# Kernel optimization log

Measured on AMD Instinct MI355X. Metric: run time of the kernel, lower is better.

Reference implementation:

```python
import jax, jax.numpy as jnp
import numpy as np

DIM = 512
LEAF_DIM = 128
DEPTH = 3
NUM_LEAVES = 2 ** DEPTH  # 8
B, T = 4, 2048


def setup_inputs() -> dict:
    key = jax.random.key(0)
    ks = jax.random.split(key, 16)
    sD = DIM ** -0.5
    sF = LEAF_DIM ** -0.5
    inp = {
        "inputs": jax.random.normal(ks[0], (B, T, DIM), jnp.float32),
        "training": 1,
    }
    # per-level node (routing) params: (D, 2^d)
    for d in range(DEPTH):
        n = 2 ** d
        inp[f"wn{d}"] = jax.random.normal(ks[1 + d], (DIM, n), jnp.float32) * sD
        inp[f"bn{d}"] = jnp.zeros((n,), jnp.float32)
    # stacked leaf FFN params
    inp["w1a"] = jax.random.normal(ks[8], (NUM_LEAVES, DIM, LEAF_DIM), jnp.float32) * sD
    inp["b1a"] = jnp.zeros((NUM_LEAVES, LEAF_DIM), jnp.float32)
    inp["w1b"] = jax.random.normal(ks[9], (NUM_LEAVES, DIM, LEAF_DIM), jnp.float32) * sD
    inp["b1b"] = jnp.zeros((NUM_LEAVES, LEAF_DIM), jnp.float32)
    inp["w2"] = jax.random.normal(ks[10], (NUM_LEAVES, LEAF_DIM, DIM), jnp.float32) * sF
    inp["b2"] = jnp.zeros((NUM_LEAVES, DIM), jnp.float32)
    return inp


def reference(inputs, training, wn0, bn0, wn1, bn1, wn2, bn2, w1a, b1a, w1b, b1b, w2, b2):
    Bs, Ts, D = inputs.shape
    L = NUM_LEAVES
    sg = jax.lax.stop_gradient
    mixture = jnp.ones((Bs, Ts, L), inputs.dtype)
    for wn, bn in ((wn0, bn0), (wn1, bn1), (wn2, bn2)):
        n = wn.shape[1]  # nodes at this depth
        c = jax.nn.sigmoid(inputs @ wn + bn)  # (B,T,n)
        if training:
            # straight-through hard rounding
            c = c - sg(c) + sg(jnp.rint(c))
        else:
            c = jnp.rint(c)
        c_nc = jnp.stack([c, 1.0 - c], -1).reshape(Bs, Ts, 2 * n, 1)
        mixture = (mixture.reshape(Bs, Ts, 2 * n, L // (2 * n)) * c_nc)
    mixture = mixture.reshape(Bs, Ts, L)
    # dense per-leaf gated FFN, masked by mixture
    h = (jnp.einsum('btd,ldf->btlf', inputs, w1a) + b1a) * \
        (jnp.einsum('btd,ldf->btlf', inputs, w1b) + b1b)  # (B,T,L,F)
    y2 = jnp.einsum('btlf,lfd->btld', h, w2) + b2          # (B,T,L,D)
    y = (y2 * mixture[..., None]).sum(-2)                  # (B,T,D)
    return y
```

## Files before the change

### kernel.cpp

```cpp
#include <hip/hip_runtime.h>
#include <hip/hip_bf16.h>

#define N_TOK 8192
#define DIM   512
#define FDIM  128
#define BM    32

typedef __attribute__((ext_vector_type(8))) short short8;
typedef __attribute__((ext_vector_type(4))) float floatx4;

__device__ inline short f2bf(float f) {
    union { float f; unsigned u; } v; v.f = f;
    unsigned r = (v.u + 0x7FFF + ((v.u >> 16) & 1)) >> 16;
    return (short)r;
}

__global__ __launch_bounds__(256) void k_prep(
    const float* __restrict__ x,
    const float* __restrict__ wn0, const float* __restrict__ bn0,
    const float* __restrict__ wn1, const float* __restrict__ bn1,
    const float* __restrict__ wn2, const float* __restrict__ bn2,
    const float* __restrict__ w1a, const float* __restrict__ w1b,
    const float* __restrict__ w2,
    int* __restrict__ counts, int* __restrict__ lists,
    short* __restrict__ pw1a, short* __restrict__ pw1b, short* __restrict__ pw2,
    short* __restrict__ xbf)
{
    const int blk = blockIdx.x;
    if (blk < 128) {
        __shared__ int leafs[64];
        const int t = threadIdx.x;
        const int wave = t >> 6, lane = t & 63;
        const int d0 = lane * 8;
        float v0[8], v1[16], v2[32];
        #pragma unroll
        for (int j = 0; j < 8; ++j)  v0[j] = wn0[d0 + j];
        #pragma unroll
        for (int j = 0; j < 16; ++j) v1[j] = wn1[d0 * 2 + j];
        #pragma unroll
        for (int j = 0; j < 32; ++j) v2[j] = wn2[d0 * 4 + j];
        const float b0s = bn0[0];
        const float b1s[2] = {bn1[0], bn1[1]};
        const float b2s[4] = {bn2[0], bn2[1], bn2[2], bn2[3]};
        for (int i = 0; i < 16; ++i) {
            const int tok = blk * 64 + wave * 16 + i;
            const float4* xp = (const float4*)(x + tok * DIM + d0);
            const float4 xa = xp[0], xb = xp[1];
            const float xv[8] = {xa.x, xa.y, xa.z, xa.w, xb.x, xb.y, xb.z, xb.w};
            short8 xo;
            #pragma unroll
            for (int j = 0; j < 8; ++j) xo[j] = f2bf(xv[j]);
            *(short8*)(xbf + (size_t)tok * DIM + d0) = xo;
            float a0 = 0.f, a1[2] = {0.f, 0.f}, a2[4] = {0.f, 0.f, 0.f, 0.f};
            #pragma unroll
            for (int j = 0; j < 8; ++j) {
                a0    += xv[j] * v0[j];
                a1[0] += xv[j] * v1[j * 2];     a1[1] += xv[j] * v1[j * 2 + 1];
                a2[0] += xv[j] * v2[j * 4];     a2[1] += xv[j] * v2[j * 4 + 1];
                a2[2] += xv[j] * v2[j * 4 + 2]; a2[3] += xv[j] * v2[j * 4 + 3];
            }
            #pragma unroll
            for (int off = 32; off >= 1; off >>= 1) {
                a0    += __shfl_xor(a0, off, 64);
                a1[0] += __shfl_xor(a1[0], off, 64);
                a1[1] += __shfl_xor(a1[1], off, 64);
                a2[0] += __shfl_xor(a2[0], off, 64);
                a2[1] += __shfl_xor(a2[1], off, 64);
                a2[2] += __shfl_xor(a2[2], off, 64);
                a2[3] += __shfl_xor(a2[3], off, 64);
            }
            int p = (a0 + b0s > 0.f) ? 0 : 1;
            const float t1 = a1[p] + b1s[p];
            p = p * 2 + ((t1 > 0.f) ? 0 : 1);
            const float t2 = a2[p] + b2s[p];
            p = p * 2 + ((t2 > 0.f) ? 0 : 1);
            if (lane == 0) leafs[wave * 16 + i] = p;
        }
        __syncthreads();
        if (t < 8) {
            const int l = t;
            int c = 0;
            for (int i = 0; i < 64; ++i) c += (leafs[i] == l);
            if (c > 0) {
                int base = atomicAdd(counts + l * 16, c);
                int j = 0;
                for (int i = 0; i < 64; ++i)
                    if (leafs[i] == l) lists[l * N_TOK + base + (j++)] = blk * 64 + i;
            }
        }
    } else {
        const int wid  = (blk - 128) * 4 + (threadIdx.x >> 6);
        const int lane = threadIdx.x & 63;
        const int q = lane >> 4, m = lane & 15;
        if (wid < 2048) {
            const float* src = (wid < 1024) ? w1a : w1b;
            short*       dst = (wid < 1024) ? pw1a : pw1b;
            const int f = wid & 1023;
            const int l = f >> 7, kb = (f >> 3) & 15, nt = f & 7;
            const float* s = src + l * 65536 + (kb * 32 + q * 8) * FDIM + nt * 16 + m;
            short8 o;
            #pragma unroll
            for (int j = 0; j < 8; ++j) o[j] = f2bf(s[j * FDIM]);
            *(short8*)(dst + f * 512 + lane * 8) = o;
        } else {
            const int f = wid - 2048;
            const int l = f >> 7, kb = (f >> 5) & 3, nt = f & 31;
            const float* s = w2 + l * 65536 + (kb * 32 + q * 8) * DIM + nt * 16 + m;
            short8 o;
            #pragma unroll
            for (int j = 0; j < 8; ++j) o[j] = f2bf(s[j * DIM]);
            *(short8*)(pw2 + f * 512 + lane * 8) = o;
        }
    }
}

__global__ __launch_bounds__(512, 4) void k_ffn(
    const short* __restrict__ xbf,
    const float* __restrict__ b1a, const float* __restrict__ b1b,
    const float* __restrict__ b2,
    const short* __restrict__ pw1a, const short* __restrict__ pw1b,
    const short* __restrict__ pw2,
    const int* __restrict__ counts, const int* __restrict__ lists,
    float* __restrict__ out)
{
    const int leaf = blockIdx.y;
    const int tile = blockIdx.x;
    const int cnt  = counts[leaf * 16];
    if (tile * BM >= cnt) return;

    __shared__ int   toks[BM];
    __shared__ short xs[BM][DIM + 8];
    __shared__ short hs[BM][FDIM + 8];

    const int t = threadIdx.x;
    if (t < BM) {
        const int idx = tile * BM + t;
        toks[t] = lists[leaf * N_TOK + ((idx < cnt) ? idx : cnt - 1)];
    }
    __syncthreads();

    {
        const int row = t >> 4, c0 = (t & 15) * 32;
        const short8* src = (const short8*)(xbf + (size_t)toks[row] * DIM + c0);
        const short8 s0 = src[0], s1 = src[1], s2 = src[2], s3 = src[3];
        short8* dst = (short8*)&xs[row][c0];
        dst[0] = s0; dst[1] = s1; dst[2] = s2; dst[3] = s3;
    }
    __syncthreads();

    const int wave = t >> 6, lane = t & 63;
    const int qd = lane >> 4, mm = lane & 15;

    floatx4 aA0 = {0,0,0,0}, aA1 = {0,0,0,0}, aB0 = {0,0,0,0}, aB1 = {0,0,0,0};
    const short* pa = pw1a + ((leaf * 16) * 8 + wave) * 512 + lane * 8;
    const short* pb = pw1b + ((leaf * 16) * 8 + wave) * 512 + lane * 8;
    #pragma unroll
    for (int kb = 0; kb < 16; ++kb) {
        const short8 af0 = *(const short8*)&xs[mm][kb * 32 + qd * 8];
        const short8 af1 = *(const short8*)&xs[16 + mm][kb * 32 + qd * 8];
        const short8 ba  = *(const short8*)(pa + kb * (8 * 512));
        const short8 bb  = *(const short8*)(pb + kb * (8 * 512));
        aA0 = __builtin_amdgcn_mfma_f32_16x16x32_bf16(af0, ba, aA0, 0, 0, 0);
        aA1 = __builtin_amdgcn_mfma_f32_16x16x32_bf16(af1, ba, aA1, 0, 0, 0);
        aB0 = __builtin_amdgcn_mfma_f32_16x16x32_bf16(af0, bb, aB0, 0, 0, 0);
        aB1 = __builtin_amdgcn_mfma_f32_16x16x32_bf16(af1, bb, aB1, 0, 0, 0);
    }
    {
        const int c0 = wave * 16 + mm;
        const float ba_ = b1a[leaf * FDIM + c0];
        const float bb_ = b1b[leaf * FDIM + c0];
        #pragma unroll
        for (int r = 0; r < 4; ++r) {
            const int r0 = qd * 4 + r;
            hs[r0][c0]      = f2bf((aA0[r] + ba_) * (aB0[r] + bb_));
            hs[16 + r0][c0] = f2bf((aA1[r] + ba_) * (aB1[r] + bb_));
        }
    }
    __syncthreads();

    floatx4 acc[8];
    #pragma unroll
    for (int j = 0; j < 8; ++j) acc[j] = (floatx4){0, 0, 0, 0};
    #pragma unroll
    for (int kb = 0; kb < 4; ++kb) {
        const short8 af0 = *(const short8*)&hs[mm][kb * 32 + qd * 8];
        const short8 af1 = *(const short8*)&hs[16 + mm][kb * 32 + qd * 8];
        #pragma unroll
        for (int j = 0; j < 4; ++j) {
            const int nt = wave * 4 + j;
            const short8 bf = *(const short8*)(pw2 + (((leaf * 4 + kb) * 32 + nt) * 512) + lane * 8);
            acc[j * 2]     = __builtin_amdgcn_mfma_f32_16x16x32_bf16(af0, bf, acc[j * 2],     0, 0, 0);
            acc[j * 2 + 1] = __builtin_amdgcn_mfma_f32_16x16x32_bf16(af1, bf, acc[j * 2 + 1], 0, 0, 0);
        }
    }
    const int rem = cnt - tile * BM;
    #pragma unroll
    for (int j = 0; j < 4; ++j) {
        const int col = (wave * 4 + j) * 16 + mm;
        const float bias = b2[leaf * DIM + col];
        #pragma unroll
        for (int r = 0; r < 4; ++r) {
            const int r0 = qd * 4 + r;
            if (r0 < rem)      out[toks[r0] * DIM + col]      = acc[j * 2][r]     + bias;
            if (16 + r0 < rem) out[toks[16 + r0] * DIM + col] = acc[j * 2 + 1][r] + bias;
        }
    }
}

extern "C" void kernel_launch(void* const* d_in, const int* in_sizes, int n_in,
                              void* d_out, int out_size, void* d_ws, size_t ws_size,
                              hipStream_t stream) {
    const float* x   = (const float*)d_in[0];
    const float* wn0 = (const float*)d_in[2];
    const float* bn0 = (const float*)d_in[3];
    const float* wn1 = (const float*)d_in[4];
    const float* bn1 = (const float*)d_in[5];
    const float* wn2 = (const float*)d_in[6];
    const float* bn2 = (const float*)d_in[7];
    const float* w1a = (const float*)d_in[8];
    const float* b1a = (const float*)d_in[9];
    const float* w1b = (const float*)d_in[10];
    const float* b1b = (const float*)d_in[11];
    const float* w2  = (const float*)d_in[12];
    const float* b2  = (const float*)d_in[13];
    float* out = (float*)d_out;

    char* ws = (char*)d_ws;
    int*   counts = (int*)(ws);
    int*   lists  = (int*)(ws + 512);
    short* pw1a   = (short*)(ws + 262656);
    short* pw1b   = (short*)(ws + 262656 + 1048576);
    short* pw2    = (short*)(ws + 262656 + 2097152);
    short* xbf    = (short*)(ws + 262656 + 3145728);

    hipMemsetAsync(counts, 0, 512, stream);
    k_prep<<<896, 256, 0, stream>>>(x, wn0, bn0, wn1, bn1, wn2, bn2,
                                    w1a, w1b, w2, counts, lists, pw1a, pw1b, pw2, xbf);
    k_ffn<<<dim3(256, 8), 512, 0, stream>>>(xbf, b1a, b1b, b2, pw1a, pw1b, pw2,
                                            counts, lists, out);
}
```

Baseline: 135.7 us.

## Fuse routing prep and leaf FFN into one cooperative persistent kernel

Merges the prep kernel (routing, bf16 conversion, weight packing) and the FFN kernel into a single cooperative launch of 256 blocks. A grid-wide sync separates the two phases. The FFN phase then pulls tiles from an atomic work queue instead of launching a sparse 256x8 grid with many early-exit blocks. This removes one kernel launch and the idle blocks, but adds grid-sync cost, queue atomics, and a lower occupancy bound of 2 blocks per CU.

```diff
diff --git a/kernel.cpp b/kernel.cpp
--- a/kernel.cpp
+++ b/kernel.cpp
@@ -1,5 +1,7 @@
 #include <hip/hip_runtime.h>
-#include <hip/hip_bf16.h>
+#include <hip/hip_cooperative_groups.h>
+
+namespace cg = cooperative_groups;
 
 #define N_TOK 8192
 #define DIM   512
@@ -15,22 +17,31 @@
     return (short)r;
 }
 
-__global__ __launch_bounds__(256) void k_prep(
+__global__ __launch_bounds__(512, 2) void k_fused(
     const float* __restrict__ x,
     const float* __restrict__ wn0, const float* __restrict__ bn0,
     const float* __restrict__ wn1, const float* __restrict__ bn1,
     const float* __restrict__ wn2, const float* __restrict__ bn2,
     const float* __restrict__ w1a, const float* __restrict__ w1b,
     const float* __restrict__ w2,
-    int* __restrict__ counts, int* __restrict__ lists,
+    const float* __restrict__ b1a, const float* __restrict__ b1b,
+    const float* __restrict__ b2,
+    int* __restrict__ counts, int* __restrict__ lists, int* __restrict__ queue,
     short* __restrict__ pw1a, short* __restrict__ pw1b, short* __restrict__ pw2,
-    short* __restrict__ xbf)
+    short* __restrict__ xbf,
+    float* __restrict__ out)
 {
-    const int blk = blockIdx.x;
-    if (blk < 128) {
-        __shared__ int leafs[64];
-        const int t = threadIdx.x;
-        const int wave = t >> 6, lane = t & 63;
+    const int blk  = blockIdx.x;
+    const int t    = threadIdx.x;
+    const int wave = t >> 6, lane = t & 63;
+
+    __shared__ int   sleafs[32];
+    __shared__ int   toks[BM];
+    __shared__ short xs[BM][DIM + 8];
+    __shared__ short hs[BM][FDIM + 8];
+    __shared__ int   s_it;
+
+    if (wave < 4) {
         const int d0 = lane * 8;
         float v0[8], v1[16], v2[32];
         #pragma unroll
@@ -42,8 +53,9 @@
         const float b0s = bn0[0];
         const float b1s[2] = {bn1[0], bn1[1]};
         const float b2s[4] = {bn2[0], bn2[1], bn2[2], bn2[3]};
-        for (int i = 0; i < 16; ++i) {
-            const int tok = blk * 64 + wave * 16 + i;
+        #pragma unroll 2
+        for (int i = 0; i < 8; ++i) {
+            const int tok = blk * 32 + wave * 8 + i;
             const float4* xp = (const float4*)(x + tok * DIM + d0);
             const float4 xa = xp[0], xb = xp[1];
             const float xv[8] = {xa.x, xa.y, xa.z, xa.w, xb.x, xb.y, xb.z, xb.w};
@@ -74,136 +86,136 @@
             p = p * 2 + ((t1 > 0.f) ? 0 : 1);
             const float t2 = a2[p] + b2s[p];
             p = p * 2 + ((t2 > 0.f) ? 0 : 1);
-            if (lane == 0) leafs[wave * 16 + i] = p;
-        }
-        __syncthreads();
-        if (t < 8) {
-            const int l = t;
-            int c = 0;
-            for (int i = 0; i < 64; ++i) c += (leafs[i] == l);
-            if (c > 0) {
-                int base = atomicAdd(counts + l * 16, c);
-                int j = 0;
-                for (int i = 0; i < 64; ++i)
-                    if (leafs[i] == l) lists[l * N_TOK + base + (j++)] = blk * 64 + i;
-            }
+            if (lane == 0) sleafs[wave * 8 + i] = p;
         }
     } else {
-        const int wid  = (blk - 128) * 4 + (threadIdx.x >> 6);
-        const int lane = threadIdx.x & 63;
+        const int wglob = blk * 4 + (wave - 4);
         const int q = lane >> 4, m = lane & 15;
-        if (wid < 2048) {
-            const float* src = (wid < 1024) ? w1a : w1b;
-            short*       dst = (wid < 1024) ? pw1a : pw1b;
-            const int f = wid & 1023;
-            const int l = f >> 7, kb = (f >> 3) & 15, nt = f & 7;
-            const float* s = src + l * 65536 + (kb * 32 + q * 8) * FDIM + nt * 16 + m;
-            short8 o;
-            #pragma unroll
-            for (int j = 0; j < 8; ++j) o[j] = f2bf(s[j * FDIM]);
-            *(short8*)(dst + f * 512 + lane * 8) = o;
-        } else {
-            const int f = wid - 2048;
-            const int l = f >> 7, kb = (f >> 5) & 3, nt = f & 31;
-            const float* s = w2 + l * 65536 + (kb * 32 + q * 8) * DIM + nt * 16 + m;
-            short8 o;
-            #pragma unroll
-            for (int j = 0; j < 8; ++j) o[j] = f2bf(s[j * DIM]);
-            *(short8*)(pw2 + f * 512 + lane * 8) = o;
-        }
-    }
-}
-
-__global__ __launch_bounds__(512, 4) void k_ffn(
-    const short* __restrict__ xbf,
-    const float* __restrict__ b1a, const float* __restrict__ b1b,
-    const float* __restrict__ b2,
-    const short* __restrict__ pw1a, const short* __restrict__ pw1b,
-    const short* __restrict__ pw2,
-    const int* __restrict__ counts, const int* __restrict__ lists,
-    float* __restrict__ out)
-{
-    const int leaf = blockIdx.y;
-    const int tile = blockIdx.x;
-    const int cnt  = counts[leaf * 16];
-    if (tile * BM >= cnt) return;
-
-    __shared__ int   toks[BM];
-    __shared__ short xs[BM][DIM + 8];
-    __shared__ short hs[BM][FDIM + 8];
-
-    const int t = threadIdx.x;
-    if (t < BM) {
-        const int idx = tile * BM + t;
-        toks[t] = lists[leaf * N_TOK + ((idx < cnt) ? idx : cnt - 1)];
+        #pragma unroll
+        for (int u = 0; u < 3; ++u) {
+            const int wid = wglob * 3 + u;
+            if (wid < 2048) {
+                const float* src = (wid < 1024) ? w1a : w1b;
+                short*       dst = (wid < 1024) ? pw1a : pw1b;
+                const int f = wid & 1023;
+                const int l = f >> 7, kb = (f >> 3) & 15, nt = f & 7;
+                const float* s = src + l * 65536 + (kb * 32 + q * 8) * FDIM + nt * 16 + m;
+                short8 o;
+                #pragma unroll
+                for (int j = 0; j < 8; ++j) o[j] = f2bf(s[j * FDIM]);
+                *(short8*)(dst + f * 512 + lane * 8) = o;
+            } else {
+                const int f = wid - 2048;
+                const int l = f >> 7, kb = (f >> 5) & 3, nt = f & 31;
+                const float* s = w2 + l * 65536 + (kb * 32 + q * 8) * DIM + nt * 16 + m;
+                short8 o;
+                #pragma unroll
+                for (int j = 0; j < 8; ++j) o[j] = f2bf(s[j * DIM]);
+                *(short8*)(pw2 + f * 512 + lane * 8) = o;
+            }
+        }
     }
     __syncthreads();
-
-    {
-        const int row = t >> 4, c0 = (t & 15) * 32;
-        const short8* src = (const short8*)(xbf + (size_t)toks[row] * DIM + c0);
-        const short8 s0 = src[0], s1 = src[1], s2 = src[2], s3 = src[3];
-        short8* dst = (short8*)&xs[row][c0];
-        dst[0] = s0; dst[1] = s1; dst[2] = s2; dst[3] = s3;
+    if (t < 8) {
+        const int l = t;
+        int c = 0;
+        for (int i = 0; i < 32; ++i) c += (sleafs[i] == l);
+        if (c > 0) {
+            int base = atomicAdd(counts + l * 16, c);
+            int j = 0;
+            for (int i = 0; i < 32; ++i)
+                if (sleafs[i] == l) lists[l * N_TOK + base + (j++)] = blk * 32 + i;
+        }
     }
-    __syncthreads();
-
-    const int wave = t >> 6, lane = t & 63;
+
+    cg::this_grid().sync();
+
+    int pre[8]; int tot = 0;
+    #pragma unroll
+    for (int l = 0; l < 8; ++l) { pre[l] = tot; tot += (counts[l * 16] + BM - 1) / BM; }
+
     const int qd = lane >> 4, mm = lane & 15;
-
-    floatx4 aA0 = {0,0,0,0}, aA1 = {0,0,0,0}, aB0 = {0,0,0,0}, aB1 = {0,0,0,0};
-    const short* pa = pw1a + ((leaf * 16) * 8 + wave) * 512 + lane * 8;
-    const short* pb = pw1b + ((leaf * 16) * 8 + wave) * 512 + lane * 8;
-    #pragma unroll
-    for (int kb = 0; kb < 16; ++kb) {
-        const short8 af0 = *(const short8*)&xs[mm][kb * 32 + qd * 8];
-        const short8 af1 = *(const short8*)&xs[16 + mm][kb * 32 + qd * 8];
-        const short8 ba  = *(const short8*)(pa + kb * (8 * 512));
-        const short8 bb  = *(const short8*)(pb + kb * (8 * 512));
-        aA0 = __builtin_amdgcn_mfma_f32_16x16x32_bf16(af0, ba, aA0, 0, 0, 0);
-        aA1 = __builtin_amdgcn_mfma_f32_16x16x32_bf16(af1, ba, aA1, 0, 0, 0);
-        aB0 = __builtin_amdgcn_mfma_f32_16x16x32_bf16(af0, bb, aB0, 0, 0, 0);
-        aB1 = __builtin_amdgcn_mfma_f32_16x16x32_bf16(af1, bb, aB1, 0, 0, 0);
-    }
-    {
-        const int c0 = wave * 16 + mm;
-        const float ba_ = b1a[leaf * FDIM + c0];
-        const float bb_ = b1b[leaf * FDIM + c0];
-        #pragma unroll
-        for (int r = 0; r < 4; ++r) {
-            const int r0 = qd * 4 + r;
-            hs[r0][c0]      = f2bf((aA0[r] + ba_) * (aB0[r] + bb_));
-            hs[16 + r0][c0] = f2bf((aA1[r] + ba_) * (aB1[r] + bb_));
-        }
-    }
-    __syncthreads();
-
-    floatx4 acc[8];
-    #pragma unroll
-    for (int j = 0; j < 8; ++j) acc[j] = (floatx4){0, 0, 0, 0};
-    #pragma unroll
-    for (int kb = 0; kb < 4; ++kb) {
-        const short8 af0 = *(const short8*)&hs[mm][kb * 32 + qd * 8];
-        const short8 af1 = *(const short8*)&hs[16 + mm][kb * 32 + qd * 8];
+    for (;;) {
+        if (t == 0) s_it = atomicAdd(queue, 1);
+        __syncthreads();
+        const int it = s_it;
+        if (it >= tot) break;
+        int leaf = 0;
+        #pragma unroll
+        for (int l = 1; l < 8; ++l) if (it >= pre[l]) leaf = l;
+        const int tile = it - pre[leaf];
+        const int cnt  = counts[leaf * 16];
+
+        if (t < BM) {
+            const int idx = tile * BM + t;
+            toks[t] = lists[leaf * N_TOK + ((idx < cnt) ? idx : cnt - 1)];
+        }
+        __syncthreads();
+
+        {
+            const int row = t >> 4, c0 = (t & 15) * 32;
+            const short8* src = (const short8*)(xbf + (size_t)toks[row] * DIM + c0);
+            const short8 s0 = src[0], s1 = src[1], s2 = src[2], s3 = src[3];
+            short8* dst = (short8*)&xs[row][c0];
+            dst[0] = s0; dst[1] = s1; dst[2] = s2; dst[3] = s3;
+        }
+        __syncthreads();
+
+        floatx4 aA0 = {0,0,0,0}, aA1 = {0,0,0,0}, aB0 = {0,0,0,0}, aB1 = {0,0,0,0};
+        const short* pa = pw1a + ((leaf * 16) * 8 + wave) * 512 + lane * 8;
+        const short* pb = pw1b + ((leaf * 16) * 8 + wave) * 512 + lane * 8;
+        #pragma unroll
+        for (int kb = 0; kb < 16; ++kb) {
+            const short8 af0 = *(const short8*)&xs[mm][kb * 32 + qd * 8];
+            const short8 af1 = *(const short8*)&xs[16 + mm][kb * 32 + qd * 8];
+            const short8 ba  = *(const short8*)(pa + kb * (8 * 512));
+            const short8 bb  = *(const short8*)(pb + kb * (8 * 512));
+            aA0 = __builtin_amdgcn_mfma_f32_16x16x32_bf16(af0, ba, aA0, 0, 0, 0);
+            aA1 = __builtin_amdgcn_mfma_f32_16x16x32_bf16(af1, ba, aA1, 0, 0, 0);
+            aB0 = __builtin_amdgcn_mfma_f32_16x16x32_bf16(af0, bb, aB0, 0, 0, 0);
+            aB1 = __builtin_amdgcn_mfma_f32_16x16x32_bf16(af1, bb, aB1, 0, 0, 0);
+        }
+        {
+            const int c0 = wave * 16 + mm;
+            const float ba_ = b1a[leaf * FDIM + c0];
+            const float bb_ = b1b[leaf * FDIM + c0];
+            #pragma unroll
+            for (int r = 0; r < 4; ++r) {
+                const int r0 = qd * 4 + r;
+                hs[r0][c0]      = f2bf((aA0[r] + ba_) * (aB0[r] + bb_));
+                hs[16 + r0][c0] = f2bf((aA1[r] + ba_) * (aB1[r] + bb_));
+            }
+        }
+        __syncthreads();
+
+        floatx4 acc[8];
+        #pragma unroll
+        for (int j = 0; j < 8; ++j) acc[j] = (floatx4){0, 0, 0, 0};
+        #pragma unroll
+        for (int kb = 0; kb < 4; ++kb) {
+            const short8 af0 = *(const short8*)&hs[mm][kb * 32 + qd * 8];
+            const short8 af1 = *(const short8*)&hs[16 + mm][kb * 32 + qd * 8];
+            #pragma unroll
+            for (int j = 0; j < 4; ++j) {
+                const int nt = wave * 4 + j;
+                const short8 bf = *(const short8*)(pw2 + (((leaf * 4 + kb) * 32 + nt) * 512) + lane * 8);
+                acc[j * 2]     = __builtin_amdgcn_mfma_f32_16x16x32_bf16(af0, bf, acc[j * 2],     0, 0, 0);
+                acc[j * 2 + 1] = __builtin_amdgcn_mfma_f32_16x16x32_bf16(af1, bf, acc[j * 2 + 1], 0, 0, 0);
+            }
+        }
+        const int rem = cnt - tile * BM;
         #pragma unroll
         for (int j = 0; j < 4; ++j) {
-            const int nt = wave * 4 + j;
-            const short8 bf = *(const short8*)(pw2 + (((leaf * 4 + kb) * 32 + nt) * 512) + lane * 8);
-            acc[j * 2]     = __builtin_amdgcn_mfma_f32_16x16x32_bf16(af0, bf, acc[j * 2],     0, 0, 0);
-            acc[j * 2 + 1] = __builtin_amdgcn_mfma_f32_16x16x32_bf16(af1, bf, acc[j * 2 + 1], 0, 0, 0);
-        }
-    }
-    const int rem = cnt - tile * BM;
-    #pragma unroll
-    for (int j = 0; j < 4; ++j) {
-        const int col = (wave * 4 + j) * 16 + mm;
-        const float bias = b2[leaf * DIM + col];
-        #pragma unroll
-        for (int r = 0; r < 4; ++r) {
-            const int r0 = qd * 4 + r;
-            if (r0 < rem)      out[toks[r0] * DIM + col]      = acc[j * 2][r]     + bias;
-            if (16 + r0 < rem) out[toks[16 + r0] * DIM + col] = acc[j * 2 + 1][r] + bias;
-        }
+            const int col = (wave * 4 + j) * 16 + mm;
+            const float bias = b2[leaf * DIM + col];
+            #pragma unroll
+            for (int r = 0; r < 4; ++r) {
+                const int r0 = qd * 4 + r;
+                if (r0 < rem)      out[toks[r0] * DIM + col]      = acc[j * 2][r]     + bias;
+                if (16 + r0 < rem) out[toks[16 + r0] * DIM + col] = acc[j * 2 + 1][r] + bias;
+            }
+        }
+        __syncthreads();
     }
 }
 
@@ -227,6 +239,7 @@
 
     char* ws = (char*)d_ws;
     int*   counts = (int*)(ws);
+    int*   queue  = (int*)(ws + 480);
     int*   lists  = (int*)(ws + 512);
     short* pw1a   = (short*)(ws + 262656);
     short* pw1b   = (short*)(ws + 262656 + 1048576);
@@ -234,8 +247,14 @@
     short* xbf    = (short*)(ws + 262656 + 3145728);
 
     hipMemsetAsync(counts, 0, 512, stream);
-    k_prep<<<896, 256, 0, stream>>>(x, wn0, bn0, wn1, bn1, wn2, bn2,
-                                    w1a, w1b, w2, counts, lists, pw1a, pw1b, pw2, xbf);
-    k_ffn<<<dim3(256, 8), 512, 0, stream>>>(xbf, b1a, b1b, b2, pw1a, pw1b, pw2,
-                                            counts, lists, out);
+
+    void* args[] = {
+        (void*)&x, (void*)&wn0, (void*)&bn0, (void*)&wn1, (void*)&bn1,
+        (void*)&wn2, (void*)&bn2, (void*)&w1a, (void*)&w1b, (void*)&w2,
+        (void*)&b1a, (void*)&b1b, (void*)&b2,
+        (void*)&counts, (void*)&lists, (void*)&queue,
+        (void*)&pw1a, (void*)&pw1b, (void*)&pw2, (void*)&xbf, (void*)&out
+    };
+    hipLaunchCooperativeKernel((const void*)k_fused, dim3(256), dim3(512),
+                               args, 0, stream);
 }
```

New measurement: 185.7 us. 36.8% more time.
